# Performance work log

Hardware: AMD Instinct MI355X
Metric: run time of the kernel (lower is better)

## Reference

```python
import jax, jax.numpy as jnp
import numpy as np

N_GRID = 16       # n
CELL_SIDE = 2.0
LATENT = 16       # latent_dim (pooling_dim for type_='social')
HIDDEN = 128
OUT_DIM = 128
CONSTANT = 0.0
NUM_TRACKS = 1024


def setup_inputs() -> dict:
    key = jax.random.key(0)
    ks = jax.random.split(key, 6)
    T = NUM_TRACKS
    hidden_state = jax.random.normal(ks[0], (T, HIDDEN), jnp.float32)
    # positions spread over a ~20m scene; obs2 is obs1 plus a small step (velocity)
    obs1 = jax.random.uniform(ks[1], (T, 2), jnp.float32) * 20.0
    obs2 = obs1 + jax.random.normal(ks[2], (T, 2), jnp.float32) * 0.5
    W_enc = jax.random.normal(ks[3], (HIDDEN, LATENT), jnp.float32) / np.sqrt(HIDDEN)
    b_enc = jnp.zeros((LATENT,), jnp.float32)
    in_dim = N_GRID * N_GRID * LATENT  # 4096
    W_emb = jax.random.normal(ks[4], (in_dim, OUT_DIM), jnp.float32) / np.sqrt(in_dim)
    b_emb = jnp.zeros((OUT_DIM,), jnp.float32)
    return dict(hidden_state=hidden_state, obs1=obs1, obs2=obs2,
                W_enc=W_enc, b_enc=b_enc, W_emb=W_emb, b_emb=b_emb)


def _social_grid(hidden_state, obs2, W_enc, b_enc):
    T = obs2.shape[0]
    # NaN rows -> 0 (mask = isnan(obs).any(dim=1))
    obs = jnp.where(jnp.isnan(obs2).any(axis=1, keepdims=True), 0.0, obs2)
    # static off-diagonal neighbor indices: row i lists all j != i  [T, T-1]
    cols = np.broadcast_to(np.arange(T), (T, T))
    nbr = cols[~np.eye(T, dtype=bool)].reshape(T, T - 1)
    rel = obs[nbr] - obs[:, None, :]                 # [T, T-1, 2] obs[j]-obs[i]
    vals = hidden_state[nbr] @ W_enc + b_enc         # [T, T-1, LATENT]
    # grid cell coordinates (pool_size=1, front=False)
    oij = rel / CELL_SIDE + N_GRID / 2.0             # [T, T-1, 2]
    in_range = jnp.sum((oij < 0) | (oij >= N_GRID), axis=2) == 0  # [T, T-1]
    oij_i = jnp.where(in_range[..., None], oij, 0.0).astype(jnp.int32)
    vals = jnp.where(in_range[..., None], vals, CONSTANT)
    oi = oij_i[..., 0] * N_GRID + oij_i[..., 1]      # flat cell index [T, T-1]
    occ = jnp.full((T, N_GRID * N_GRID, LATENT), CONSTANT, vals.dtype)
    occ = occ.at[jnp.arange(T)[:, None], oi].set(vals)
    # [T, LATENT, n, n]; blur_size=1 and lp_pool with kernel=pool_size=1 are identity
    return jnp.transpose(occ, (0, 2, 1)).reshape(T, LATENT, N_GRID, N_GRID)


def reference(hidden_state, obs1, obs2, W_enc, b_enc, W_emb, b_emb):
    grid = _social_grid(hidden_state, obs2, W_enc, b_enc)
    T = grid.shape[0]
    flat = grid.reshape(T, -1)                       # [T, n*n*LATENT]
    return jax.nn.relu(flat @ W_emb + b_emb)         # [T, OUT_DIM]
```

## Files before the change

### kernel.cpp

```cpp
#include <hip/hip_runtime.h>
#include <hip/hip_bf16.h>
#include <math.h>

#define T_TRACKS 1024
#define HIDDEN 128
#define LATENT 16
#define NGRID 16
#define NCELLS 256
#define KDIM 4096
#define OUTD 128

typedef unsigned short ushort_t;
typedef __attribute__((ext_vector_type(8))) short frag_ab;
typedef __attribute__((ext_vector_type(4))) float f32x4;

static __device__ inline ushort_t f2bf(float x) {
    __hip_bfloat16 h = __float2bfloat16(x);
    return *reinterpret_cast<ushort_t*>(&h);
}

#define WS_VALS 0
#define WS_WT   32768
#define WS_OCC  1081344
#define WS_ACC  9469952
#define WS_NEED 9994240

__global__ __launch_bounds__(256) void prep_kernel(const float* __restrict__ hidden,
                                                   const float* __restrict__ W_enc,
                                                   const float* __restrict__ b_enc,
                                                   const float* __restrict__ W_emb,
                                                   ushort_t* __restrict__ vals_bf16,
                                                   ushort_t* __restrict__ W_t,
                                                   float* __restrict__ accum) {
    const int b = blockIdx.x;
    const int tid = threadIdx.x;
    if (b < 64) {
        int idx = b * 256 + tid;
        int j = idx >> 4, l = idx & 15;
        const float* h = hidden + j * HIDDEN;
        float acc = b_enc[l];
#pragma unroll 8
        for (int k = 0; k < HIDDEN; k++) acc += h[k] * W_enc[k * LATENT + l];
        vals_bf16[idx] = f2bf(acc);
    } else if (b < 320) {
        int idx = (b - 64) * 256 + tid;
        int kc = idx >> 7;
        int o = idx & 127;
        ushort_t tmp[8];
#pragma unroll
        for (int u = 0; u < 8; u++) tmp[u] = f2bf(W_emb[(kc * 8 + u) * OUTD + o]);
        *reinterpret_cast<uint4*>(W_t + o * KDIM + kc * 8) = *reinterpret_cast<uint4*>(tmp);
    } else {
        int idx = (b - 320) * 256 + tid;
        float4 z; z.x = z.y = z.z = z.w = 0.0f;
        reinterpret_cast<float4*>(accum)[idx] = z;
    }
}

__global__ __launch_bounds__(256) void occ_kernel(const float* __restrict__ obs2,
                                                  const ushort_t* __restrict__ vals_bf16,
                                                  ushort_t* __restrict__ occ) {
    const int i = blockIdx.x;
    const int tid = threadIdx.x;
    __shared__ int owner[NCELLS];
    owner[tid] = -1;

    float oix = obs2[i * 2 + 0];
    float oiy = obs2[i * 2 + 1];
    if (isnan(oix) || isnan(oiy)) { oix = 0.0f; oiy = 0.0f; }
    __syncthreads();

    for (int j = tid; j < T_TRACKS; j += 256) {
        if (j == i) continue;
        float ox = obs2[j * 2 + 0];
        float oy = obs2[j * 2 + 1];
        if (isnan(ox) || isnan(oy)) { ox = 0.0f; oy = 0.0f; }
        float gx = (ox - oix) * 0.5f + 8.0f;
        float gy = (oy - oiy) * 0.5f + 8.0f;
        bool inr = (gx >= 0.0f) && (gx < 16.0f) && (gy >= 0.0f) && (gy < 16.0f);
        int c = inr ? ((int)gx * NGRID + (int)gy) : 0;
        atomicMax(&owner[c], j);
    }
    __syncthreads();

    const int l = tid >> 4;
    const int cbase = (tid & 15) * 16;
    ushort_t outv[16];
#pragma unroll
    for (int u = 0; u < 16; u++) {
        int c = cbase + u;
        int j = owner[c];
        bool valid = (j >= 0);
        if (c == 0 && valid) {
            float ox = obs2[j * 2 + 0];
            float oy = obs2[j * 2 + 1];
            if (isnan(ox) || isnan(oy)) { ox = 0.0f; oy = 0.0f; }
            float gx = (ox - oix) * 0.5f + 8.0f;
            float gy = (oy - oiy) * 0.5f + 8.0f;
            valid = (gx >= 0.0f) && (gx < 16.0f) && (gy >= 0.0f) && (gy < 16.0f);
        }
        int jj = (j >= 0) ? j : 0;
        outv[u] = valid ? vals_bf16[jj * LATENT + l] : (ushort_t)0;
    }
    uint4* dst = reinterpret_cast<uint4*>(occ + i * KDIM + tid * 16);
    dst[0] = reinterpret_cast<uint4*>(outv)[0];
    dst[1] = reinterpret_cast<uint4*>(outv)[1];
}

#define BK 128
#define LDSTR 136
__global__ __launch_bounds__(256) void gemm_kernel(const ushort_t* __restrict__ occ,
                                                   const ushort_t* __restrict__ W_t,
                                                   float* __restrict__ accum) {
    const int tid = threadIdx.x;
    const int kt = blockIdx.x & 15;
    const int mt = blockIdx.x >> 4;
    const int wave = tid >> 6;
    const int lane = tid & 63;
    const int lrow = lane & 15;
    const int quad = lane >> 4;

    __shared__ ushort_t As[64 * LDSTR];
    __shared__ ushort_t Bs[128 * LDSTR];

    f32x4 acc[8];
#pragma unroll
    for (int nt = 0; nt < 8; nt++) acc[nt] = (f32x4){0.f, 0.f, 0.f, 0.f};

    for (int chunk = 0; chunk < 2; chunk++) {
        const int k0 = kt * 256 + chunk * BK;
        for (int g = tid; g < 1024; g += 256) {
            int r = g >> 4, cs = g & 15;
            uint4 v = *reinterpret_cast<const uint4*>(occ + (mt * 64 + r) * KDIM + k0 + cs * 8);
            *reinterpret_cast<uint4*>(As + r * LDSTR + cs * 8) = v;
        }
        for (int g = tid; g < 2048; g += 256) {
            int n = g >> 4, cs = g & 15;
            uint4 v = *reinterpret_cast<const uint4*>(W_t + n * KDIM + k0 + cs * 8);
            *reinterpret_cast<uint4*>(Bs + n * LDSTR + cs * 8) = v;
        }
        __syncthreads();
#pragma unroll
        for (int ks = 0; ks < 4; ks++) {
            const int koff = ks * 32 + quad * 8;
            frag_ab a = *reinterpret_cast<const frag_ab*>(&As[(wave * 16 + lrow) * LDSTR + koff]);
#pragma unroll
            for (int nt = 0; nt < 8; nt++) {
                frag_ab bfr = *reinterpret_cast<const frag_ab*>(&Bs[(nt * 16 + lrow) * LDSTR + koff]);
                acc[nt] = __builtin_amdgcn_mfma_f32_16x16x32_bf16(a, bfr, acc[nt], 0, 0, 0);
            }
        }
        __syncthreads();
    }
#pragma unroll
    for (int nt = 0; nt < 8; nt++) {
        int n = nt * 16 + lrow;
#pragma unroll
        for (int reg = 0; reg < 4; reg++) {
            int m = mt * 64 + wave * 16 + quad * 4 + reg;
            atomicAdd(&accum[m * OUTD + n], acc[nt][reg]);
        }
    }
}

__global__ __launch_bounds__(256) void epilogue_kernel(const float* __restrict__ accum,
                                                       const float* __restrict__ b_emb,
                                                       float* __restrict__ out) {
    int idx = blockIdx.x * 256 + threadIdx.x;
    float4 v = reinterpret_cast<const float4*>(accum)[idx];
    float4 bv = reinterpret_cast<const float4*>(b_emb)[idx & 31];
    float4 r;
    r.x = fmaxf(v.x + bv.x, 0.0f);
    r.y = fmaxf(v.y + bv.y, 0.0f);
    r.z = fmaxf(v.z + bv.z, 0.0f);
    r.w = fmaxf(v.w + bv.w, 0.0f);
    reinterpret_cast<float4*>(out)[idx] = r;
}

__global__ __launch_bounds__(256) void vals_kernel_f32(const float* __restrict__ hidden,
                                                       const float* __restrict__ W_enc,
                                                       const float* __restrict__ b_enc,
                                                       float* __restrict__ vals) {
    int idx = blockIdx.x * 256 + threadIdx.x;
    int j = idx >> 4, l = idx & 15;
    const float* h = hidden + j * HIDDEN;
    float acc = b_enc[l];
#pragma unroll 8
    for (int k = 0; k < HIDDEN; k++) acc += h[k] * W_enc[k * LATENT + l];
    vals[idx] = acc;
}

__global__ __launch_bounds__(256) void pool_kernel_f32(const float* __restrict__ obs2,
                                                       const float* __restrict__ vals,
                                                       const float* __restrict__ W_emb,
                                                       const float* __restrict__ b_emb,
                                                       float* __restrict__ out) {
    const int i = blockIdx.x;
    const int tid = threadIdx.x;
    __shared__ int owner[NCELLS];
    __shared__ float occ[NCELLS * LATENT];
    __shared__ float partial[OUTD];
    owner[tid] = -1;
    float oix = obs2[i * 2 + 0];
    float oiy = obs2[i * 2 + 1];
    if (isnan(oix) || isnan(oiy)) { oix = 0.0f; oiy = 0.0f; }
    __syncthreads();
    for (int j = tid; j < T_TRACKS; j += 256) {
        if (j == i) continue;
        float ox = obs2[j * 2 + 0], oy = obs2[j * 2 + 1];
        if (isnan(ox) || isnan(oy)) { ox = 0.0f; oy = 0.0f; }
        float gx = (ox - oix) * 0.5f + 8.0f;
        float gy = (oy - oiy) * 0.5f + 8.0f;
        bool inr = (gx >= 0.0f) && (gx < 16.0f) && (gy >= 0.0f) && (gy < 16.0f);
        int c = inr ? ((int)gx * NGRID + (int)gy) : 0;
        atomicMax(&owner[c], j);
    }
    __syncthreads();
    {
        int j = owner[tid];
        bool valid = false;
        if (j >= 0) {
            float ox = obs2[j * 2 + 0], oy = obs2[j * 2 + 1];
            if (isnan(ox) || isnan(oy)) { ox = 0.0f; oy = 0.0f; }
            float gx = (ox - oix) * 0.5f + 8.0f;
            float gy = (oy - oiy) * 0.5f + 8.0f;
            valid = (gx >= 0.0f) && (gx < 16.0f) && (gy >= 0.0f) && (gy < 16.0f);
        }
        const float* vj = vals + (j >= 0 ? j : 0) * LATENT;
#pragma unroll
        for (int l = 0; l < LATENT; l++) occ[tid * LATENT + l] = valid ? vj[l] : 0.0f;
    }
    __syncthreads();
    const int o = tid & (OUTD - 1);
    const int half = tid >> 7;
    const int cbase = half * 128;
    float acc = 0.0f;
    for (int c = cbase; c < cbase + 128; c++) {
#pragma unroll
        for (int l = 0; l < LATENT; l++)
            acc += occ[c * LATENT + l] * W_emb[(l * NCELLS + c) * OUTD + o];
    }
    if (half == 0) partial[o] = acc;
    __syncthreads();
    if (half == 1) out[i * OUTD + o] = fmaxf(acc + partial[o] + b_emb[o], 0.0f);
}

extern "C" void kernel_launch(void* const* d_in, const int* in_sizes, int n_in,
                              void* d_out, int out_size, void* d_ws, size_t ws_size,
                              hipStream_t stream) {
    const float* hidden = (const float*)d_in[0];
    const float* obs2   = (const float*)d_in[2];
    const float* W_enc  = (const float*)d_in[3];
    const float* b_enc  = (const float*)d_in[4];
    const float* W_emb  = (const float*)d_in[5];
    const float* b_emb  = (const float*)d_in[6];
    float* out = (float*)d_out;

    if (ws_size < (size_t)WS_NEED) {
        float* vals = (float*)d_ws;
        vals_kernel_f32<<<(T_TRACKS * LATENT) / 256, 256, 0, stream>>>(hidden, W_enc, b_enc, vals);
        pool_kernel_f32<<<T_TRACKS, 256, 0, stream>>>(obs2, vals, W_emb, b_emb, out);
        return;
    }

    char* ws = (char*)d_ws;
    ushort_t* vals_bf16 = (ushort_t*)(ws + WS_VALS);
    ushort_t* W_t       = (ushort_t*)(ws + WS_WT);
    ushort_t* occ       = (ushort_t*)(ws + WS_OCC);
    float*    accum     = (float*)(ws + WS_ACC);

    prep_kernel<<<448, 256, 0, stream>>>(hidden, W_enc, b_enc, W_emb, vals_bf16, W_t, accum);
    occ_kernel<<<T_TRACKS, 256, 0, stream>>>(obs2, vals_bf16, occ);
    gemm_kernel<<<256, 256, 0, stream>>>(occ, W_t, accum);
    epilogue_kernel<<<128, 256, 0, stream>>>(accum, b_emb, out);
}
```

Before: 93.56 us.

## Replace atomic split-K accumulation with partial buffers and stage occ writes via LDS

The GEMM no longer uses float atomicAdd into a zeroed accumulator. Each K-split writes its own partial tile, and a reduce kernel sums the 16 partials, then adds the bias and applies ReLU. This removes the accumulator-zeroing blocks in prep and the atomic contention. The occupancy kernel now gives each thread one cell: it loads the neighbor's 16 latents with vector loads, transposes them through shared memory, then writes coalesced 16-byte stores. The trade-off is an extra 8 MB partial buffer that the reduce kernel writes and reads back.

```diff
diff --git a/kernel.cpp b/kernel.cpp
--- a/kernel.cpp
+++ b/kernel.cpp
@@ -22,16 +22,15 @@
 #define WS_VALS 0
 #define WS_WT   32768
 #define WS_OCC  1081344
-#define WS_ACC  9469952
-#define WS_NEED 9994240
+#define WS_PART 9469952
+#define WS_NEED (9469952 + 8388608)
 
 __global__ __launch_bounds__(256) void prep_kernel(const float* __restrict__ hidden,
                                                    const float* __restrict__ W_enc,
                                                    const float* __restrict__ b_enc,
                                                    const float* __restrict__ W_emb,
                                                    ushort_t* __restrict__ vals_bf16,
-                                                   ushort_t* __restrict__ W_t,
-                                                   float* __restrict__ accum) {
+                                                   ushort_t* __restrict__ W_t) {
     const int b = blockIdx.x;
     const int tid = threadIdx.x;
     if (b < 64) {
@@ -42,7 +41,7 @@
 #pragma unroll 8
         for (int k = 0; k < HIDDEN; k++) acc += h[k] * W_enc[k * LATENT + l];
         vals_bf16[idx] = f2bf(acc);
-    } else if (b < 320) {
+    } else {
         int idx = (b - 64) * 256 + tid;
         int kc = idx >> 7;
         int o = idx & 127;
@@ -50,10 +49,6 @@
 #pragma unroll
         for (int u = 0; u < 8; u++) tmp[u] = f2bf(W_emb[(kc * 8 + u) * OUTD + o]);
         *reinterpret_cast<uint4*>(W_t + o * KDIM + kc * 8) = *reinterpret_cast<uint4*>(tmp);
-    } else {
-        int idx = (b - 320) * 256 + tid;
-        float4 z; z.x = z.y = z.z = z.w = 0.0f;
-        reinterpret_cast<float4*>(accum)[idx] = z;
     }
 }
 
@@ -63,6 +58,7 @@
     const int i = blockIdx.x;
     const int tid = threadIdx.x;
     __shared__ int owner[NCELLS];
+    __shared__ ushort_t socc[LATENT * NCELLS];
     owner[tid] = -1;
 
     float oix = obs2[i * 2 + 0];
@@ -83,12 +79,8 @@
     }
     __syncthreads();
 
-    const int l = tid >> 4;
-    const int cbase = (tid & 15) * 16;
-    ushort_t outv[16];
-#pragma unroll
-    for (int u = 0; u < 16; u++) {
-        int c = cbase + u;
+    {
+        const int c = tid;
         int j = owner[c];
         bool valid = (j >= 0);
         if (c == 0 && valid) {
@@ -100,18 +92,27 @@
             valid = (gx >= 0.0f) && (gx < 16.0f) && (gy >= 0.0f) && (gy < 16.0f);
         }
         int jj = (j >= 0) ? j : 0;
-        outv[u] = valid ? vals_bf16[jj * LATENT + l] : (ushort_t)0;
-    }
-    uint4* dst = reinterpret_cast<uint4*>(occ + i * KDIM + tid * 16);
-    dst[0] = reinterpret_cast<uint4*>(outv)[0];
-    dst[1] = reinterpret_cast<uint4*>(outv)[1];
+        ushort_t vv[16];
+        *reinterpret_cast<uint4*>(vv)     = *reinterpret_cast<const uint4*>(vals_bf16 + jj * LATENT);
+        *reinterpret_cast<uint4*>(vv + 8) = *reinterpret_cast<const uint4*>(vals_bf16 + jj * LATENT + 8);
+#pragma unroll
+        for (int l = 0; l < LATENT; l++) {
+            socc[l * NCELLS + c] = valid ? vv[l] : (ushort_t)0;
+        }
+    }
+    __syncthreads();
+
+    uint4* dst = reinterpret_cast<uint4*>(occ + i * KDIM);
+    const uint4* src = reinterpret_cast<const uint4*>(socc);
+    dst[tid]       = src[tid];
+    dst[tid + 256] = src[tid + 256];
 }
 
 #define BK 128
 #define LDSTR 136
 __global__ __launch_bounds__(256) void gemm_kernel(const ushort_t* __restrict__ occ,
                                                    const ushort_t* __restrict__ W_t,
-                                                   float* __restrict__ accum) {
+                                                   float* __restrict__ partial) {
     const int tid = threadIdx.x;
     const int kt = blockIdx.x & 15;
     const int mt = blockIdx.x >> 4;
@@ -152,28 +153,35 @@
         }
         __syncthreads();
     }
+    float* pt = partial + (size_t)kt * (T_TRACKS * OUTD) + (mt * 64) * OUTD;
 #pragma unroll
     for (int nt = 0; nt < 8; nt++) {
         int n = nt * 16 + lrow;
 #pragma unroll
         for (int reg = 0; reg < 4; reg++) {
-            int m = mt * 64 + wave * 16 + quad * 4 + reg;
-            atomicAdd(&accum[m * OUTD + n], acc[nt][reg]);
-        }
-    }
-}
-
-__global__ __launch_bounds__(256) void epilogue_kernel(const float* __restrict__ accum,
-                                                       const float* __restrict__ b_emb,
-                                                       float* __restrict__ out) {
+            int m = wave * 16 + quad * 4 + reg;
+            pt[m * OUTD + n] = acc[nt][reg];
+        }
+    }
+}
+
+__global__ __launch_bounds__(256) void reduce_kernel(const float* __restrict__ partial,
+                                                     const float* __restrict__ b_emb,
+                                                     float* __restrict__ out) {
     int idx = blockIdx.x * 256 + threadIdx.x;
-    float4 v = reinterpret_cast<const float4*>(accum)[idx];
+    const float4* p4 = reinterpret_cast<const float4*>(partial);
+    float4 s = p4[idx];
+#pragma unroll
+    for (int kt = 1; kt < 16; kt++) {
+        float4 v = p4[kt * 32768 + idx];
+        s.x += v.x; s.y += v.y; s.z += v.z; s.w += v.w;
+    }
     float4 bv = reinterpret_cast<const float4*>(b_emb)[idx & 31];
     float4 r;
-    r.x = fmaxf(v.x + bv.x, 0.0f);
-    r.y = fmaxf(v.y + bv.y, 0.0f);
-    r.z = fmaxf(v.z + bv.z, 0.0f);
-    r.w = fmaxf(v.w + bv.w, 0.0f);
+    r.x = fmaxf(s.x + bv.x, 0.0f);
+    r.y = fmaxf(s.y + bv.y, 0.0f);
+    r.z = fmaxf(s.z + bv.z, 0.0f);
+    r.w = fmaxf(s.w + bv.w, 0.0f);
     reinterpret_cast<float4*>(out)[idx] = r;
 }
 
@@ -267,10 +275,10 @@
     ushort_t* vals_bf16 = (ushort_t*)(ws + WS_VALS);
     ushort_t* W_t       = (ushort_t*)(ws + WS_WT);
     ushort_t* occ       = (ushort_t*)(ws + WS_OCC);
-    float*    accum     = (float*)(ws + WS_ACC);
-
-    prep_kernel<<<448, 256, 0, stream>>>(hidden, W_enc, b_enc, W_emb, vals_bf16, W_t, accum);
+    float*    partial   = (float*)(ws + WS_PART);
+
+    prep_kernel<<<320, 256, 0, stream>>>(hidden, W_enc, b_enc, W_emb, vals_bf16, W_t);
     occ_kernel<<<T_TRACKS, 256, 0, stream>>>(obs2, vals_bf16, occ);
-    gemm_kernel<<<256, 256, 0, stream>>>(occ, W_t, accum);
-    epilogue_kernel<<<128, 256, 0, stream>>>(accum, b_emb, out);
-}
+    gemm_kernel<<<256, 256, 0, stream>>>(occ, W_t, partial);
+    reduce_kernel<<<128, 256, 0, stream>>>(partial, b_emb, out);
+}
```

Result: faster. 89.98 us (-3.8%).
